# Performance work log

Hardware: AMD Instinct MI355X
Metric: run time of the kernel (lower is better)

## Reference

```python
import jax, jax.numpy as jnp
import numpy as np

EMBED_DIM = 1024
NUM_HEADS = 16
HEAD_DIM = EMBED_DIM // NUM_HEADS
FF_DIM = 4096
B, T, S = 2, 2048, 2048
LN_EPS = 1e-5


def setup_inputs() -> dict:
    key = jax.random.key(0)
    ks = jax.random.split(key, 20)
    sd = 1.0 / np.sqrt(EMBED_DIM)
    d = {
        'x': jax.random.normal(ks[0], (B, T, EMBED_DIM), jnp.float32),
        'encoder_outputs': jax.random.normal(ks[1], (B, S, EMBED_DIM), jnp.float32),
        'tgt_mask': jnp.tril(jnp.ones((T, T), bool))[None, None],  # [1,1,T,T] causal
    }
    # weights stored [in, out] so y = x @ W + b
    names = ['sa_wq', 'sa_wk', 'sa_wv', 'sa_wo', 'ca_wq', 'ca_wk', 'ca_wv', 'ca_wo']
    for i, n in enumerate(names):
        d[n] = jax.random.normal(ks[2 + i], (EMBED_DIM, EMBED_DIM), jnp.float32) * sd
        d[n.replace('w', 'b')] = jnp.zeros((EMBED_DIM,), jnp.float32)
    d['ff_w1'] = jax.random.normal(ks[10], (EMBED_DIM, FF_DIM), jnp.float32) * sd
    d['ff_b1'] = jnp.zeros((FF_DIM,), jnp.float32)
    d['ff_w2'] = jax.random.normal(ks[11], (FF_DIM, EMBED_DIM), jnp.float32) * (1.0 / np.sqrt(FF_DIM))
    d['ff_b2'] = jnp.zeros((EMBED_DIM,), jnp.float32)
    for i in (1, 2, 3):
        d[f'ln{i}_g'] = jnp.ones((EMBED_DIM,), jnp.float32)
        d[f'ln{i}_b'] = jnp.zeros((EMBED_DIM,), jnp.float32)
    return d


def _layernorm(x, g, b):
    mu = jnp.mean(x, -1, keepdims=True)
    var = jnp.mean(jnp.square(x - mu), -1, keepdims=True)
    return (x - mu) * jax.lax.rsqrt(var + LN_EPS) * g + b


def _mha(q_in, k_in, v_in, wq, bq, wk, bk, wv, bv, wo, bo, mask=None):
    Bq, Tq, C = q_in.shape
    Tk = k_in.shape[1]
    Q = (q_in @ wq + bq).reshape(Bq, Tq, NUM_HEADS, HEAD_DIM)
    K = (k_in @ wk + bk).reshape(Bq, Tk, NUM_HEADS, HEAD_DIM)
    V = (v_in @ wv + bv).reshape(Bq, Tk, NUM_HEADS, HEAD_DIM)
    scores = jnp.einsum('bqhd,bkhd->bhqk', Q, K) / np.sqrt(HEAD_DIM)
    if mask is not None:
        scores = jnp.where(mask, scores, -jnp.inf)
    attn = jax.nn.softmax(scores, axis=-1)
    out = jnp.einsum('bhqk,bkhd->bqhd', attn, V).reshape(Bq, Tq, C)
    return out @ wo + bo


def reference(x, encoder_outputs, tgt_mask,
              sa_wq, sa_bq, sa_wk, sa_bk, sa_wv, sa_bv, sa_wo, sa_bo,
              ca_wq, ca_bq, ca_wk, ca_bk, ca_wv, ca_bv, ca_wo, ca_bo,
              ff_w1, ff_b1, ff_w2, ff_b2,
              ln1_g, ln1_b, ln2_g, ln2_b, ln3_g, ln3_b):
    h = _layernorm(x, ln1_g, ln1_b)
    x = x + _mha(h, h, h, sa_wq, sa_bq, sa_wk, sa_bk, sa_wv, sa_bv, sa_wo, sa_bo, tgt_mask)
    h = _layernorm(x, ln2_g, ln2_b)
    x = x + _mha(h, encoder_outputs, encoder_outputs,
                 ca_wq, ca_bq, ca_wk, ca_bk, ca_wv, ca_bv, ca_wo, ca_bo, None)
    h = _layernorm(x, ln3_g, ln3_b)
    ff = jax.nn.relu(h @ ff_w1 + ff_b1) @ ff_w2 + ff_b2
    return x + ff
```

## Files before the change

kernel.cpp:

```cpp
#include <hip/hip_runtime.h>
#include <stdint.h>


typedef __bf16 bf16x8 __attribute__((ext_vector_type(8)));
typedef float  f32x4  __attribute__((ext_vector_type(4)));

#define T_SEQ 2048
#define NROWS 4096
#define QSCALE 0.18033688011112042f

__device__ __forceinline__ unsigned short f2bf(float f) {
  union { float f; unsigned int u; } v; v.f = f;
  unsigned int u = v.u;
  return (unsigned short)((u + 0x7FFFu + ((u >> 16) & 1u)) >> 16);
}
__device__ __forceinline__ float bf2f(unsigned short h) {
  union { unsigned int u; float f; } v; v.u = ((unsigned int)h) << 16;
  return v.f;
}
__device__ __forceinline__ unsigned int pk2(float a, float b) {
  return (unsigned int)f2bf(a) | ((unsigned int)f2bf(b) << 16);
}
__device__ __forceinline__ unsigned int pk2t(float a, float b) {
  union { float f; unsigned int u; } ua, ub;
  ua.f = a; ub.f = b;
  return __builtin_amdgcn_perm(ub.u, ua.u, 0x07060302u);
}
__device__ __forceinline__ float fexp2(float x) {
  return __builtin_amdgcn_exp2f(x);
}
union U4 { unsigned int u[4]; bf16x8 v; };

__global__ void probe_dtype_kernel(const unsigned short* __restrict__ p,
                                   int* __restrict__ flag) {
  __shared__ int cnt;
  if (threadIdx.x == 0) cnt = 0;
  __syncthreads();
  int bad = 0;
  for (int i = threadIdx.x; i < 4096; i += 256) {
    unsigned short u = p[i];
    int e = (u >> 7) & 0xFF;
    if (u != 0 && (e < 100 || e > 140)) bad++;
  }
  atomicAdd(&cnt, bad);
  __syncthreads();
  if (threadIdx.x == 0) *flag = (cnt < 512) ? 1 : 0;
}

struct WTbl {
  const void* src[10];
  int K[10], N[10], start[10];
  unsigned int dstoff[10];
};
__global__ void wtrans_fused_kernel(WTbl tbl, unsigned short* __restrict__ wsbase,
                                    const int* __restrict__ flag) {
  __shared__ unsigned short tile[32][33];
  const int lb = blockIdx.x;
  int wi = 0;
#pragma unroll
  for (int i = 1; i < 10; i++) wi = (lb >= tbl.start[i]) ? i : wi;
  const int local = lb - tbl.start[wi];
  const int Nw = tbl.N[wi], Kw = tbl.K[wi];
  const int bx = local & ((Nw >> 5) - 1);
  const int by = local / (Nw >> 5);
  const void* W = tbl.src[wi];
  unsigned short* Wt = wsbase + tbl.dstoff[wi];
  const int n0 = bx * 32, k0 = by * 32;
  const int c = threadIdx.x & 31, r0 = threadIdx.x >> 5;
  const bool isbf = (*flag != 0);
  for (int r = r0; r < 32; r += 8) {
    unsigned short v;
    if (isbf) v = ((const unsigned short*)W)[(size_t)(k0 + r) * Nw + n0 + c];
    else      v = f2bf(((const float*)W)[(size_t)(k0 + r) * Nw + n0 + c]);
    tile[r][c] = v;
  }
  __syncthreads();
  const bool packed = (wi == 3) || (wi >= 7);
  if (!packed) {
    for (int r = r0; r < 32; r += 8)
      Wt[(size_t)(n0 + r) * Kw + k0 + c] = tile[c][r];
  } else {
    const int k = k0 + c;
    const size_t kpart = ((size_t)(k >> 5) << 9) + ((((k >> 3) & 3) << 7) + (k & 7));
    const size_t kfr = (size_t)(Kw >> 5);
    for (int r = r0; r < 32; r += 8) {
      const int n = n0 + r;
      Wt[((size_t)(n >> 4) * kfr << 9) + kpart + ((n & 15) << 3)] = tile[c][r];
    }
  }
}

struct PTbl { const void* p[19]; };
__global__ void param_cvt_kernel(PTbl tbl, float* __restrict__ out,
                                 const int* __restrict__ flag) {
  const int blk = blockIdx.x;
  const int off = (blk >= 8 && blk < 12) ? (blk - 8) * 1024 : 0;
  const void* src = tbl.p[blk];
  const int i = threadIdx.x * 4;
  float4 o;
  if (*flag) {
    const unsigned short* u = (const unsigned short*)src + off;
    ushort4 q = *(const ushort4*)&u[i];
    o.x = bf2f(q.x); o.y = bf2f(q.y); o.z = bf2f(q.z); o.w = bf2f(q.w);
  } else {
    o = *(const float4*)&((const float*)src)[off + i];
  }
  *(float4*)&out[blk * 1024 + i] = o;
}

__global__ void cvt_to_bf16_kernel(const void* __restrict__ in,
                                   unsigned short* __restrict__ out,
                                   int n, const int* __restrict__ flag) {
  int i = (blockIdx.x * 256 + threadIdx.x) * 8;
  if (i >= n) return;
  if (*flag) {
    *(int4*)&out[i] = *(const int4*)&((const unsigned short*)in)[i];
  } else {
    const float* f = (const float*)in;
    float4 a = *(const float4*)&f[i];
    float4 c = *(const float4*)&f[i + 4];
    ushort4 o1, o2;
    o1.x = f2bf(a.x); o1.y = f2bf(a.y); o1.z = f2bf(a.z); o1.w = f2bf(a.w);
    o2.x = f2bf(c.x); o2.y = f2bf(c.y); o2.z = f2bf(c.z); o2.w = f2bf(c.w);
    *(ushort4*)&out[i] = o1;
    *(ushort4*)&out[i + 4] = o2;
  }
}

__global__ void cvt_to_f32_kernel(const void* __restrict__ in,
                                  float* __restrict__ out,
                                  int n, const int* __restrict__ flag) {
  int i = (blockIdx.x * 256 + threadIdx.x) * 4;
  if (i >= n) return;
  if (*flag) {
    const unsigned short* u = (const unsigned short*)in;
    ushort4 q = *(const ushort4*)&u[i];
    float4 o;
    o.x = bf2f(q.x); o.y = bf2f(q.y); o.z = bf2f(q.z); o.w = bf2f(q.w);
    *(float4*)&out[i] = o;
  } else {
    *(float4*)&out[i] = *(const float4*)&((const float*)in)[i];
  }
}

__global__ __launch_bounds__(256) void ln_kernel(
    const float* __restrict__ x, const float* __restrict__ g,
    const float* __restrict__ b, unsigned short* __restrict__ out) {
  const int row = blockIdx.x;
  const int t = threadIdx.x;
  const size_t base = (size_t)row * 1024;
  float4 v = *(const float4*)&x[base + t * 4];
  float s1 = v.x + v.y + v.z + v.w;
  float s2 = v.x * v.x + v.y * v.y + v.z * v.z + v.w * v.w;
#pragma unroll
  for (int d = 1; d < 64; d <<= 1) {
    s1 += __shfl_xor(s1, d, 64);
    s2 += __shfl_xor(s2, d, 64);
  }
  __shared__ float a1[4], a2[4];
  if ((t & 63) == 0) { a1[t >> 6] = s1; a2[t >> 6] = s2; }
  __syncthreads();
  s1 = a1[0] + a1[1] + a1[2] + a1[3];
  s2 = a2[0] + a2[1] + a2[2] + a2[3];
  const float mean = s1 * (1.0f / 1024.0f);
  const float var = s2 * (1.0f / 1024.0f) - mean * mean;
  const float rstd = rsqrtf(fmaxf(var, 0.0f) + 1e-5f);
  float4 gv = *(const float4*)&g[t * 4];
  float4 bv = *(const float4*)&b[t * 4];
  ushort4 o;
  o.x = f2bf((v.x - mean) * rstd * gv.x + bv.x);
  o.y = f2bf((v.y - mean) * rstd * gv.y + bv.y);
  o.z = f2bf((v.z - mean) * rstd * gv.z + bv.z);
  o.w = f2bf((v.w - mean) * rstd * gv.w + bv.w);
  *(ushort4*)&out[base + t * 4] = o;
}

template <int BM, int BN, int BK, int RELU, int RESID, int OUTM,
          int BIASROW, int SCALEMODE>
__global__ __launch_bounds__(256, 2) void gemm_kernel(
    const unsigned short* __restrict__ A, const unsigned short* __restrict__ Bt,
    const float* __restrict__ bias, const float* __restrict__ resid,
    void* __restrict__ outp, int M, int N, int K,
    const int* __restrict__ flag) {
  static_assert(BK == 64, "swizzle assumes 8 chunks/row");
  constexpr int WX = (BN == 64) ? 1 : 2;
  constexpr int WY = 4 / WX;
  constexpr int WM = BM / WY, WN = BN / WX;
  constexpr int MI = WM / 16, NJ = WN / 16;
  constexpr int ACALLS = BM * BK / 2048;
  constexpr int RPC = 2048 / BK;
  __shared__ unsigned short lsA[2][BM * BK];
  const int t = threadIdx.x;
  const int wave = t >> 6, lane = t & 63;
  const int ml = lane & 15, quad = lane >> 4;
  const int cx = ml & 7;
  const int wm = (wave / WX) * WM, wn = (wave % WX) * WN;

  const int nx = gridDim.x, ny = gridDim.y;
  const int lin = (int)blockIdx.y * nx + (int)blockIdx.x;
  const int per = 8 * nx;
  const int y0 = (lin / per) * 8;
  const int gsz = (ny - y0 < 8) ? (ny - y0) : 8;
  const int by = y0 + (lin % gsz);
  const int bx = (lin % per) / gsz;
  const size_t m0 = (size_t)by * BM;
  const size_t n0 = (size_t)bx * BN;

  f32x4 acc[MI][NJ];
  const f32x4 fz = {0.f, 0.f, 0.f, 0.f};
#pragma unroll
  for (int i = 0; i < MI; i++)
#pragma unroll
    for (int j = 0; j < NJ; j++) acc[i][j] = fz;

  const int rowL = t >> 3;
  const int colL = (((t & 7) ^ ((t >> 3) & 7)) * 8);
  const unsigned short* gA = A + (m0 + rowL) * (size_t)K + colL;
  const int kfr = K >> 5;
  const unsigned short* gBp =
      Bt + ((size_t)((n0 + wn) >> 4) * kfr) * 512 + lane * 8;

  auto stageA = [&](unsigned short* dA, int k0) {
#pragma unroll
    for (int c = 0; c < ACALLS; c++)
      __builtin_amdgcn_global_load_lds(
          (const __attribute__((address_space(1))) void*)(gA + (size_t)(c * RPC) * K + k0),
          (__attribute__((address_space(3))) void*)(dA + c * 2048 + wave * 512), 16, 0, 0);
  };
  auto loadB = [&](bf16x8 (&bq)[NJ][2], int k0) {
#pragma unroll
    for (int j = 0; j < NJ; j++)
#pragma unroll
      for (int h = 0; h < 2; h++)
        bq[j][h] = *(const bf16x8*)(gBp + ((size_t)j * kfr + (k0 >> 5) + h) * 512);
  };
  auto comp = [&](const unsigned short* bA, const bf16x8 (&bq)[NJ][2]) {
#pragma unroll
    for (int h = 0; h < 2; h++) {
      bf16x8 af[MI];
#pragma unroll
      for (int i = 0; i < MI; i++)
        af[i] = *(const bf16x8*)
            &bA[(wm + i * 16 + ml) * BK + (((h * 4 + quad) ^ cx) * 8)];
#pragma unroll
      for (int i = 0; i < MI; i++)
#pragma unroll
        for (int j = 0; j < NJ; j++)
          acc[i][j] = __builtin_amdgcn_mfma_f32_16x16x32_bf16(af[i], bq[j][h],
                                                              acc[i][j], 0, 0, 0);
    }
  };

  const int nk = K / BK;
  bf16x8 bq0[NJ][2], bq1[NJ][2];
  stageA(&lsA[0][0], 0);
  loadB(bq0, 0);
  int tk = 0;
  while (tk < nk) {
    asm volatile("s_waitcnt vmcnt(0)" ::: "memory");
    __builtin_amdgcn_s_barrier();
    if (tk + 1 < nk) { stageA(&lsA[1][0], (tk + 1) * BK); loadB(bq1, (tk + 1) * BK); }
    comp(&lsA[0][0], bq0);
    if (tk + 1 < nk) {
      asm volatile("s_waitcnt vmcnt(0)" ::: "memory");
      __builtin_amdgcn_s_barrier();
      if (tk + 2 < nk) { stageA(&lsA[0][0], (tk + 2) * BK); loadB(bq0, (tk + 2) * BK); }
      comp(&lsA[1][0], bq1);
    }
    tk += 2;
  }

  const bool obf = (OUTM == 1) || (OUTM == 2 && *flag != 0);
#pragma unroll
  for (int j = 0; j < NJ; j++) {
    const size_t cg = n0 + wn + j * 16 + ml;
    const float bcol = BIASROW ? 0.0f : bias[cg];
    const float sc = (SCALEMODE == 0) ? 1.0f
                   : (SCALEMODE == 1) ? QSCALE
                                      : (cg < 1024 ? QSCALE : 1.0f);
#pragma unroll
    for (int i = 0; i < MI; i++) {
#pragma unroll
      for (int r = 0; r < 4; r++) {
        const size_t rg = m0 + wm + i * 16 + quad * 4 + r;
        const float bval = BIASROW ? bias[rg] : bcol;
        float v = (acc[i][j][r] + bval) * sc;
        if (RELU) v = fmaxf(v, 0.0f);
        if (RESID) v += resid[rg * N + cg];
        if (obf) ((unsigned short*)outp)[rg * N + cg] = f2bf(v);
        else     ((float*)outp)[rg * N + cg] = v;
      }
    }
  }
}

struct GSeg {
  const unsigned short* A; const unsigned short* B;
  const float* bias; unsigned short* out;
  int N, K, start, gxlog2, mode;
};
template <int NSEG>
__global__ __launch_bounds__(256, 4) void gemm_multi_kernel(GSeg s0, GSeg s1,
                                                            GSeg s2) {
  constexpr int BM = 128, BN = 64, BK = 64;
  constexpr int WM = 32, WN = 64;
  constexpr int MI = 2, NJ = 4;
  __shared__ unsigned short lsA[BM * BK];
  __shared__ unsigned short lsB[BN * BK];
  const int blk = (int)blockIdx.x;
  GSeg sg = s0;
  if (NSEG > 1 && blk >= s1.start) sg = s1;
  if (NSEG > 2 && blk >= s2.start) sg = s2;
  const int t = threadIdx.x;
  const int wave = t >> 6, lane = t & 63;
  const int ml = lane & 15, quad = lane >> 4;
  const int cx = ml & 7;
  const int wm = wave * WM, wn = 0;
  const int N = sg.N, K = sg.K;

  const int lin = blk - sg.start;
  const int per = 8 << sg.gxlog2;
  const int y0 = (lin / per) * 8;
  const int by = y0 + (lin & 7);
  const int bx = (lin & (per - 1)) >> 3;
  const size_t m0 = (size_t)by * BM;
  const size_t n0 = (size_t)bx * BN;

  f32x4 acc[MI][NJ];
  const f32x4 fz = {0.f, 0.f, 0.f, 0.f};
#pragma unroll
  for (int i = 0; i < MI; i++)
#pragma unroll
    for (int j = 0; j < NJ; j++) acc[i][j] = fz;

  const int rowL = t >> 3;
  const int colL = (((t & 7) ^ ((t >> 3) & 7)) * 8);
  const unsigned short* gA = sg.A + (m0 + rowL) * (size_t)K + colL;
  const unsigned short* gB = sg.B + (n0 + rowL) * (size_t)K + colL;

  for (int k0 = 0; k0 < K; k0 += BK) {
    __syncthreads();
#pragma unroll
    for (int c = 0; c < 4; c++)
      __builtin_amdgcn_global_load_lds(
          (const __attribute__((address_space(1))) void*)(gA + (size_t)(c * 32) * K + k0),
          (__attribute__((address_space(3))) void*)&lsA[c * 2048 + wave * 512], 16, 0, 0);
#pragma unroll
    for (int c = 0; c < 2; c++)
      __builtin_amdgcn_global_load_lds(
          (const __attribute__((address_space(1))) void*)(gB + (size_t)(c * 32) * K + k0),
          (__attribute__((address_space(3))) void*)&lsB[c * 2048 + wave * 512], 16, 0, 0);
    __syncthreads();
#pragma unroll
    for (int h = 0; h < BK / 32; h++) {
      bf16x8 af[MI], bfv[NJ];
#pragma unroll
      for (int i = 0; i < MI; i++)
        af[i] = *(const bf16x8*)
            &lsA[(wm + i * 16 + ml) * BK + (((h * 4 + quad) ^ cx) * 8)];
#pragma unroll
      for (int j = 0; j < NJ; j++)
        bfv[j] = *(const bf16x8*)
            &lsB[(wn + j * 16 + ml) * BK + (((h * 4 + quad) ^ cx) * 8)];
#pragma unroll
      for (int i = 0; i < MI; i++)
#pragma unroll
        for (int j = 0; j < NJ; j++)
          acc[i][j] = __builtin_amdgcn_mfma_f32_16x16x32_bf16(af[i], bfv[j],
                                                              acc[i][j], 0, 0, 0);
    }
  }

  const int mode = sg.mode;
#pragma unroll
  for (int j = 0; j < NJ; j++) {
    const size_t cg = n0 + wn + j * 16 + ml;
    const float bcol = (mode & 1) ? 0.0f : sg.bias[cg];
    const float sc = (mode & 2) ? QSCALE
                   : ((mode & 4) && cg < 1024) ? QSCALE : 1.0f;
#pragma unroll
    for (int i = 0; i < MI; i++) {
#pragma unroll
      for (int r = 0; r < 4; r++) {
        const size_t rg = m0 + wm + i * 16 + quad * 4 + r;
        const float bval = (mode & 1) ? sg.bias[rg] : bcol;
        float v = (acc[i][j][r] + bval) * sc;
        sg.out[rg * N + cg] = f2bf(v);
      }
    }
  }
}

template <int CAUSAL>
__global__ __launch_bounds__(256, 4) void attn_kernel(
    const unsigned short* __restrict__ Q, const unsigned short* __restrict__ K,
    const unsigned short* __restrict__ VT, unsigned short* __restrict__ O,
    int qstride, int kstride) {
  __shared__ unsigned short Ks[4096];
  __shared__ unsigned short Vs[4096];
  __shared__ unsigned short Qs[4608];
  const int t = threadIdx.x;
  const int wave = t >> 6, lane = t & 63;
  const int ml = lane & 15, quad = lane >> 4;
  const int cx = ml & 7;
  const int bh = blockIdx.y, b = bh >> 4, h = bh & 15;
  const int qb = CAUSAL ? ((int)gridDim.x - 1 - (int)blockIdx.x) : (int)blockIdx.x;
  const int q0 = qb * 64;
  const int lr = lane >> 3;
  const int scol = (((lane & 7) ^ lr) * 8);

  {
    const unsigned short* g0 =
        Q + ((size_t)(b * T_SEQ + q0 + wave * 16 + lr)) * qstride + h * 64 + scol;
    __builtin_amdgcn_global_load_lds(
        (const __attribute__((address_space(1))) void*)g0,
        (__attribute__((address_space(3))) void*)&Qs[wave * 2 * 512], 16, 0, 0);
    const unsigned short* g1 = g0 + (size_t)8 * qstride;
    __builtin_amdgcn_global_load_lds(
        (const __attribute__((address_space(1))) void*)g1,
        (__attribute__((address_space(3))) void*)&Qs[(wave * 2 + 1) * 512], 16, 0, 0);
  }

  int sp_[2];
#pragma unroll
  for (int i = 0; i < 2; i++) {
    int p = (wave * 2 + i) * 8 + lr;
    sp_[i] = ((p & 16) << 1) | ((p & 12) << 1) | ((p & 32) >> 3) | (p & 3);
  }
  const unsigned short* kg0 =
      K + ((size_t)b * T_SEQ + sp_[0]) * kstride + h * 64 + scol;
  const unsigned short* kg1 =
      K + ((size_t)b * T_SEQ + sp_[1]) * kstride + h * 64 + scol;
  const unsigned short* vg0 =
      VT + ((size_t)(h * 64 + wave * 16 + lr)) * 4096 + (size_t)b * T_SEQ + scol;
  const unsigned short* vg1 = vg0 + (size_t)8 * 4096;

  __syncthreads();
  const bf16x8 aq0 = *(const bf16x8*)&Qs[(wave * 16 + ml) * 64 + ((quad ^ cx) * 8)];
  const bf16x8 aq1 = *(const bf16x8*)&Qs[(wave * 16 + ml) * 64 + (((quad + 4) ^ cx) * 8)];

  f32x4 acc[4];
  const f32x4 fz = {0.f, 0.f, 0.f, 0.f};
#pragma unroll
  for (int n = 0; n < 4; n++) acc[n] = fz;
  float m_i = -3.0e38f, l_part = 0.0f;
  const int q_glob = q0 + wave * 16 + ml;
  const int nkb = CAUSAL ? (qb + 1) : (T_SEQ / 64);
  const size_t kinc = (size_t)64 * kstride;

  for (int kb = 0; kb < nkb; kb++) {
    __syncthreads();
    __builtin_amdgcn_global_load_lds(
        (const __attribute__((address_space(1))) void*)kg0,
        (__attribute__((address_space(3))) void*)&Ks[(wave * 2) * 512], 16, 0, 0);
    __builtin_amdgcn_global_load_lds(
        (const __attribute__((address_space(1))) void*)kg1,
        (__attribute__((address_space(3))) void*)&Ks[(wave * 2 + 1) * 512], 16, 0, 0);
    __builtin_amdgcn_global_load_lds(
        (const __attribute__((address_space(1))) void*)vg0,
        (__attribute__((address_space(3))) void*)&Vs[(wave * 2) * 512], 16, 0, 0);
    __builtin_amdgcn_global_load_lds(
        (const __attribute__((address_space(1))) void*)vg1,
        (__attribute__((address_space(3))) void*)&Vs[(wave * 2 + 1) * 512], 16, 0, 0);
    kg0 += kinc; kg1 += kinc; vg0 += 64; vg1 += 64;
    __syncthreads();

    f32x4 s[4];
#pragma unroll
    for (int nt = 0; nt < 4; nt++) {
      bf16x8 k0 = *(const bf16x8*)&Ks[(nt * 16 + ml) * 64 + ((quad ^ cx) * 8)];
      bf16x8 k1 = *(const bf16x8*)&Ks[(nt * 16 + ml) * 64 + (((quad + 4) ^ cx) * 8)];
      f32x4 a = fz;
      a = __builtin_amdgcn_mfma_f32_16x16x32_bf16(k0, aq0, a, 0, 0, 0);
      a = __builtin_amdgcn_mfma_f32_16x16x32_bf16(k1, aq1, a, 0, 0, 0);
      s[nt] = a;
    }
    if (CAUSAL && kb == nkb - 1) {
#pragma unroll
      for (int nt = 0; nt < 4; nt++)
#pragma unroll
        for (int r = 0; r < 4; r++) {
          int key = kb * 64 + ((nt & 1) << 5) + (quad << 3) + ((nt >> 1) << 2) + r;
          if (key > q_glob) s[nt][r] = -3.0e38f;
        }
    }
    float tm = -3.0e38f;
#pragma unroll
    for (int nt = 0; nt < 4; nt++)
#pragma unroll
      for (int r = 0; r < 4; r++) tm = fmaxf(tm, s[nt][r]);
    tm = fmaxf(tm, __shfl_xor(tm, 16));
    tm = fmaxf(tm, __shfl_xor(tm, 32));
    if (__any(tm > m_i)) {
      const float m_new = fmaxf(m_i, tm);
      const float alpha = fexp2(m_i - m_new);
      l_part *= alpha;
#pragma unroll
      for (int n = 0; n < 4; n++)
#pragma unroll
        for (int r = 0; r < 4; r++) acc[n][r] *= alpha;
      m_i = m_new;
    }
    float p[4][4];
    float rs = 0.f;
#pragma unroll
    for (int nt = 0; nt < 4; nt++)
#pragma unroll
      for (int r = 0; r < 4; r++) {
        p[nt][r] = fexp2(s[nt][r] - m_i);
        rs += p[nt][r];
      }
    l_part += rs;

    U4 P0, P1;
    P0.u[0] = pk2t(p[0][0], p[0][1]); P0.u[1] = pk2t(p[0][2], p[0][3]);
    P0.u[2] = pk2t(p[2][0], p[2][1]); P0.u[3] = pk2t(p[2][2], p[2][3]);
    P1.u[0] = pk2t(p[1][0], p[1][1]); P1.u[1] = pk2t(p[1][2], p[1][3]);
    P1.u[2] = pk2t(p[3][0], p[3][1]); P1.u[3] = pk2t(p[3][2], p[3][3]);

#pragma unroll
    for (int n = 0; n < 4; n++) {
      bf16x8 v0 = *(const bf16x8*)&Vs[(n * 16 + ml) * 64 + ((quad ^ cx) * 8)];
      bf16x8 v1 = *(const bf16x8*)&Vs[(n * 16 + ml) * 64 + (((quad + 4) ^ cx) * 8)];
      acc[n] = __builtin_amdgcn_mfma_f32_16x16x32_bf16(v0, P0.v, acc[n], 0, 0, 0);
      acc[n] = __builtin_amdgcn_mfma_f32_16x16x32_bf16(v1, P1.v, acc[n], 0, 0, 0);
    }
  }

  float l_i = l_part;
  l_i += __shfl_xor(l_i, 16);
  l_i += __shfl_xor(l_i, 32);

  const float inv = 1.0f / l_i;
#pragma unroll
  for (int n = 0; n < 4; n++)
#pragma unroll
    for (int rp = 0; rp < 2; rp++) {
      unsigned int u = pk2(acc[n][2 * rp] * inv, acc[n][2 * rp + 1] * inv);
      *(unsigned int*)&Qs[(wave * 16 + ml) * 72 + n * 16 + quad * 4 + 2 * rp] = u;
    }
  __syncthreads();
  {
    const int q = t >> 2, d0 = (t & 3) * 16;
    unsigned short* og = O + ((size_t)(b * T_SEQ + q0 + q)) * 1024 + h * 64 + d0;
    *(int4*)og = *(const int4*)&Qs[q * 72 + d0];
    *(int4*)(og + 8) = *(const int4*)&Qs[q * 72 + d0 + 8];
  }
}

extern "C" void kernel_launch(void* const* d_in, const int* in_sizes, int n_in,
                              void* d_out, int out_size, void* d_ws,
                              size_t ws_size, hipStream_t stream) {
  (void)in_sizes; (void)n_in; (void)out_size; (void)ws_size;
  const size_t MEG = 1048576;
  unsigned short* ws16 = (unsigned short*)d_ws;
  char* wsb = (char*)d_ws;

  unsigned short* wt[10];
  for (int i = 0; i < 8; i++) wt[i] = ws16 + (size_t)i * MEG;
  wt[8] = ws16 + 8 * MEG;
  wt[9] = ws16 + 12 * MEG;
  unsigned short* encB  = ws16 + 16 * MEG;
  unsigned short* hbuf  = ws16 + 20 * MEG;
  unsigned short* QKb   = ws16 + 24 * MEG;
  unsigned short* Qb    = ws16 + 32 * MEG;
  unsigned short* Kb    = ws16 + 36 * MEG;
  unsigned short* Vb    = ws16 + 40 * MEG;
  unsigned short* attnb = ws16 + 44 * MEG;
  unsigned short* ffh   = ws16 + 24 * MEG;
  float* xf32 = (float*)(wsb + 96 * MEG);
  float* pbuf = (float*)(wsb + 112 * MEG);
  int* flag   = (int*)(wsb + 113 * MEG);

  probe_dtype_kernel<<<1, 256, 0, stream>>>((const unsigned short*)d_in[0], flag);

  {
    WTbl tb;
    const int widx[10] = {3, 5, 7, 9, 11, 13, 15, 17, 19, 21};
    int st = 0;
    for (int i = 0; i < 10; i++) {
      tb.src[i] = d_in[widx[i]];
      tb.K[i] = (i == 9) ? 4096 : 1024;
      tb.N[i] = (i == 8) ? 4096 : 1024;
      tb.start[i] = st;
      st += (tb.K[i] / 32) * (tb.N[i] / 32);
      tb.dstoff[i] = (unsigned int)((i < 8) ? i * MEG : (i == 8 ? 8 * MEG : 12 * MEG));
    }
    wtrans_fused_kernel<<<16384, 256, 0, stream>>>(tb, ws16, flag);
  }

  cvt_to_f32_kernel<<<4096, 256, 0, stream>>>(d_in[0], xf32, 4194304, flag);
  cvt_to_bf16_kernel<<<2048, 256, 0, stream>>>(d_in[1], encB, 4194304, flag);

  {
    PTbl pt;
    const int pidx[19] = {4, 6, 8, 10, 12, 14, 16, 18,
                          20, 20, 20, 20, 22, 23, 24, 25, 26, 27, 28};
    for (int i = 0; i < 19; i++) pt.p[i] = d_in[pidx[i]];
    param_cvt_kernel<<<19, 256, 0, stream>>>(pt, pbuf, flag);
  }
  float* bqk_sa = pbuf;
  float* bv_sa  = pbuf + 2048;
  float* bo_sa  = pbuf + 3072;
  float* bq_ca  = pbuf + 4096;
  float* bk_ca  = pbuf + 5120;
  float* bv_ca  = pbuf + 6144;
  float* bo_ca  = pbuf + 7168;
  float* ff_b1p = pbuf + 8192;
  float* ff_b2p = pbuf + 12288;
  float* ln1g = pbuf + 13312; float* ln1b = pbuf + 14336;
  float* ln2g = pbuf + 15360; float* ln2b = pbuf + 16384;
  float* ln3g = pbuf + 17408; float* ln3b = pbuf + 18432;

  dim3 gP(16, 32);
  dim3 gFF1(32, 32);
  dim3 gFF2(8, 64);
  dim3 gAttn(32, 32);

  ln_kernel<<<4096, 256, 0, stream>>>(xf32, ln1g, ln1b, hbuf);
  {
    GSeg sQK = {hbuf, wt[0], bqk_sa, QKb, 2048, 1024, 0, 5, 4};
    GSeg sVT = {wt[2], hbuf, bv_sa, Vb, 4096, 1024, 1024, 6, 1};
    gemm_multi_kernel<2><<<1536, 256, 0, stream>>>(sQK, sVT, sVT);
  }
  attn_kernel<1><<<gAttn, 256, 0, stream>>>(QKb, QKb + 1024, Vb, attnb, 2048, 2048);
  gemm_kernel<128, 64, 64, 0, 1, 0, 0, 0><<<gP, 256, 0, stream>>>(
      attnb, wt[3], bo_sa, xf32, xf32, NROWS, 1024, 1024, nullptr);

  ln_kernel<<<4096, 256, 0, stream>>>(xf32, ln2g, ln2b, hbuf);
  {
    GSeg sQ = {hbuf, wt[4], bq_ca, Qb, 1024, 1024, 0, 4, 2};
    GSeg sK = {encB, wt[5], bk_ca, Kb, 1024, 1024, 512, 4, 0};
    GSeg sV = {wt[6], encB, bv_ca, Vb, 4096, 1024, 1024, 6, 1};
    gemm_multi_kernel<3><<<1536, 256, 0, stream>>>(sQ, sK, sV);
  }
  attn_kernel<0><<<gAttn, 256, 0, stream>>>(Qb, Kb, Vb, attnb, 1024, 1024);
  gemm_kernel<128, 64, 64, 0, 1, 0, 0, 0><<<gP, 256, 0, stream>>>(
      attnb, wt[7], bo_ca, xf32, xf32, NROWS, 1024, 1024, nullptr);

  ln_kernel<<<4096, 256, 0, stream>>>(xf32, ln3g, ln3b, hbuf);
  gemm_kernel<128, 128, 64, 1, 0, 1, 0, 0><<<gFF1, 256, 0, stream>>>(
      hbuf, wt[8], ff_b1p, nullptr, ffh, NROWS, 4096, 1024, nullptr);
  gemm_kernel<64, 128, 64, 0, 1, 2, 0, 0><<<gFF2, 256, 0, stream>>>(
      ffh, wt[9], ff_b2p, xf32, d_out, NROWS, 1024, 4096, flag);
}
```

Before: 577.3 us.

## Double-buffer attention K/V tiles, split-K the FF2 GEMM, lazy softmax rescale

The attention kernel now double-buffers its K and V tiles in LDS, so loads for the next key block are issued before the current block is computed. The epilogue reuses the K buffer, which lets the Q staging area shrink. The online-softmax rescale now runs only when the running max grows by more than 8, cutting how often rescaling happens. Separately, FF2 is split along K into two halves that write fp32 partials, and a new combine kernel adds the partials, bias and residual. This doubles FF2 parallelism at the cost of extra partial-buffer traffic and one more launch.

Result: faster. 564.6 us (-2.2%).

```diff
diff --git a/kernel.cpp b/kernel.cpp
--- a/kernel.cpp
+++ b/kernel.cpp
@@ -176,12 +176,12 @@
 }
 
 template <int BM, int BN, int BK, int RELU, int RESID, int OUTM,
-          int BIASROW, int SCALEMODE>
+          int BIASROW, int SCALEMODE, int SPLITK>
 __global__ __launch_bounds__(256, 2) void gemm_kernel(
     const unsigned short* __restrict__ A, const unsigned short* __restrict__ Bt,
     const float* __restrict__ bias, const float* __restrict__ resid,
     void* __restrict__ outp, int M, int N, int K,
-    const int* __restrict__ flag) {
+    const int* __restrict__ flag, void* __restrict__ outp2) {
   static_assert(BK == 64, "swizzle assumes 8 chunks/row");
   constexpr int WX = (BN == 64) ? 1 : 2;
   constexpr int WY = 4 / WX;
@@ -251,23 +251,40 @@
     }
   };
 
-  const int nk = K / BK;
+  const int kbase = SPLITK ? (int)blockIdx.z * (K >> 1) : 0;
+  const int nk = (SPLITK ? (K >> 1) : K) / BK;
   bf16x8 bq0[NJ][2], bq1[NJ][2];
-  stageA(&lsA[0][0], 0);
-  loadB(bq0, 0);
+  stageA(&lsA[0][0], kbase);
+  loadB(bq0, kbase);
   int tk = 0;
   while (tk < nk) {
     asm volatile("s_waitcnt vmcnt(0)" ::: "memory");
     __builtin_amdgcn_s_barrier();
-    if (tk + 1 < nk) { stageA(&lsA[1][0], (tk + 1) * BK); loadB(bq1, (tk + 1) * BK); }
+    if (tk + 1 < nk) { stageA(&lsA[1][0], kbase + (tk + 1) * BK); loadB(bq1, kbase + (tk + 1) * BK); }
     comp(&lsA[0][0], bq0);
     if (tk + 1 < nk) {
       asm volatile("s_waitcnt vmcnt(0)" ::: "memory");
       __builtin_amdgcn_s_barrier();
-      if (tk + 2 < nk) { stageA(&lsA[0][0], (tk + 2) * BK); loadB(bq0, (tk + 2) * BK); }
+      if (tk + 2 < nk) { stageA(&lsA[0][0], kbase + (tk + 2) * BK); loadB(bq0, kbase + (tk + 2) * BK); }
       comp(&lsA[1][0], bq1);
     }
     tk += 2;
+  }
+
+  if constexpr (SPLITK) {
+    float* po = (blockIdx.z == 0) ? (float*)outp : (float*)outp2;
+#pragma unroll
+    for (int j = 0; j < NJ; j++) {
+      const size_t cg = n0 + wn + j * 16 + ml;
+#pragma unroll
+      for (int i = 0; i < MI; i++)
+#pragma unroll
+        for (int r = 0; r < 4; r++) {
+          const size_t rg = m0 + wm + i * 16 + quad * 4 + r;
+          po[rg * N + cg] = acc[i][j][r];
+        }
+    }
+    return;
   }
 
   const bool obf = (OUTM == 1) || (OUTM == 2 && *flag != 0);
@@ -291,6 +308,31 @@
         else     ((float*)outp)[rg * N + cg] = v;
       }
     }
+  }
+}
+
+__global__ __launch_bounds__(256) void ff2_combine_kernel(
+    const float* __restrict__ p0, const float* __restrict__ p1,
+    const float* __restrict__ bias, const float* __restrict__ resid,
+    void* __restrict__ out, const int* __restrict__ flag) {
+  const int row = blockIdx.x;
+  const int i = threadIdx.x * 4;
+  const size_t off = (size_t)row * 1024 + i;
+  float4 a = *(const float4*)&p0[off];
+  float4 b = *(const float4*)&p1[off];
+  float4 r = *(const float4*)&resid[off];
+  float4 bb = *(const float4*)&bias[i];
+  float4 v;
+  v.x = a.x + b.x + bb.x + r.x;
+  v.y = a.y + b.y + bb.y + r.y;
+  v.z = a.z + b.z + bb.z + r.z;
+  v.w = a.w + b.w + bb.w + r.w;
+  if (*flag) {
+    ushort4 o;
+    o.x = f2bf(v.x); o.y = f2bf(v.y); o.z = f2bf(v.z); o.w = f2bf(v.w);
+    *(ushort4*)&((unsigned short*)out)[off] = o;
+  } else {
+    *(float4*)&((float*)out)[off] = v;
   }
 }
 
@@ -396,9 +438,9 @@
     const unsigned short* __restrict__ Q, const unsigned short* __restrict__ K,
     const unsigned short* __restrict__ VT, unsigned short* __restrict__ O,
     int qstride, int kstride) {
-  __shared__ unsigned short Ks[4096];
-  __shared__ unsigned short Vs[4096];
-  __shared__ unsigned short Qs[4608];
+  __shared__ unsigned short Ks[2][4096];
+  __shared__ unsigned short Vs[2][4096];
+  __shared__ unsigned short Qs[4096];
   const int t = threadIdx.x;
   const int wave = t >> 6, lane = t & 63;
   const int ml = lane & 15, quad = lane >> 4;
@@ -434,6 +476,7 @@
   const unsigned short* vg0 =
       VT + ((size_t)(h * 64 + wave * 16 + lr)) * 4096 + (size_t)b * T_SEQ + scol;
   const unsigned short* vg1 = vg0 + (size_t)8 * 4096;
+  const size_t kinc = (size_t)64 * kstride;
 
   __syncthreads();
   const bf16x8 aq0 = *(const bf16x8*)&Qs[(wave * 16 + ml) * 64 + ((quad ^ cx) * 8)];
@@ -446,30 +489,29 @@
   float m_i = -3.0e38f, l_part = 0.0f;
   const int q_glob = q0 + wave * 16 + ml;
   const int nkb = CAUSAL ? (qb + 1) : (T_SEQ / 64);
-  const size_t kinc = (size_t)64 * kstride;
-
-  for (int kb = 0; kb < nkb; kb++) {
-    __syncthreads();
+
+  auto stage = [&](unsigned short* kdst, unsigned short* vdst) {
     __builtin_amdgcn_global_load_lds(
         (const __attribute__((address_space(1))) void*)kg0,
-        (__attribute__((address_space(3))) void*)&Ks[(wave * 2) * 512], 16, 0, 0);
+        (__attribute__((address_space(3))) void*)(kdst + (wave * 2) * 512), 16, 0, 0);
     __builtin_amdgcn_global_load_lds(
         (const __attribute__((address_space(1))) void*)kg1,
-        (__attribute__((address_space(3))) void*)&Ks[(wave * 2 + 1) * 512], 16, 0, 0);
+        (__attribute__((address_space(3))) void*)(kdst + (wave * 2 + 1) * 512), 16, 0, 0);
     __builtin_amdgcn_global_load_lds(
         (const __attribute__((address_space(1))) void*)vg0,
-        (__attribute__((address_space(3))) void*)&Vs[(wave * 2) * 512], 16, 0, 0);
+        (__attribute__((address_space(3))) void*)(vdst + (wave * 2) * 512), 16, 0, 0);
     __builtin_amdgcn_global_load_lds(
         (const __attribute__((address_space(1))) void*)vg1,
-        (__attribute__((address_space(3))) void*)&Vs[(wave * 2 + 1) * 512], 16, 0, 0);
+        (__attribute__((address_space(3))) void*)(vdst + (wave * 2 + 1) * 512), 16, 0, 0);
     kg0 += kinc; kg1 += kinc; vg0 += 64; vg1 += 64;
-    __syncthreads();
-
+  };
+
+  auto compute = [&](const unsigned short* Kb, const unsigned short* Vb, int kb) {
     f32x4 s[4];
 #pragma unroll
     for (int nt = 0; nt < 4; nt++) {
-      bf16x8 k0 = *(const bf16x8*)&Ks[(nt * 16 + ml) * 64 + ((quad ^ cx) * 8)];
-      bf16x8 k1 = *(const bf16x8*)&Ks[(nt * 16 + ml) * 64 + (((quad + 4) ^ cx) * 8)];
+      bf16x8 k0 = *(const bf16x8*)&Kb[(nt * 16 + ml) * 64 + ((quad ^ cx) * 8)];
+      bf16x8 k1 = *(const bf16x8*)&Kb[(nt * 16 + ml) * 64 + (((quad + 4) ^ cx) * 8)];
       f32x4 a = fz;
       a = __builtin_amdgcn_mfma_f32_16x16x32_bf16(k0, aq0, a, 0, 0, 0);
       a = __builtin_amdgcn_mfma_f32_16x16x32_bf16(k1, aq1, a, 0, 0, 0);
@@ -491,7 +533,7 @@
       for (int r = 0; r < 4; r++) tm = fmaxf(tm, s[nt][r]);
     tm = fmaxf(tm, __shfl_xor(tm, 16));
     tm = fmaxf(tm, __shfl_xor(tm, 32));
-    if (__any(tm > m_i)) {
+    if (__any(tm > m_i + 8.0f)) {
       const float m_new = fmaxf(m_i, tm);
       const float alpha = fexp2(m_i - m_new);
       l_part *= alpha;
@@ -520,10 +562,24 @@
 
 #pragma unroll
     for (int n = 0; n < 4; n++) {
-      bf16x8 v0 = *(const bf16x8*)&Vs[(n * 16 + ml) * 64 + ((quad ^ cx) * 8)];
-      bf16x8 v1 = *(const bf16x8*)&Vs[(n * 16 + ml) * 64 + (((quad + 4) ^ cx) * 8)];
+      bf16x8 v0 = *(const bf16x8*)&Vb[(n * 16 + ml) * 64 + ((quad ^ cx) * 8)];
+      bf16x8 v1 = *(const bf16x8*)&Vb[(n * 16 + ml) * 64 + (((quad + 4) ^ cx) * 8)];
       acc[n] = __builtin_amdgcn_mfma_f32_16x16x32_bf16(v0, P0.v, acc[n], 0, 0, 0);
       acc[n] = __builtin_amdgcn_mfma_f32_16x16x32_bf16(v1, P1.v, acc[n], 0, 0, 0);
+    }
+  };
+
+  stage(&Ks[0][0], &Vs[0][0]);
+  for (int kb = 0; kb < nkb; kb += 2) {
+    asm volatile("s_waitcnt vmcnt(0)" ::: "memory");
+    __syncthreads();
+    if (kb + 1 < nkb) stage(&Ks[1][0], &Vs[1][0]);
+    compute(&Ks[0][0], &Vs[0][0], kb);
+    if (kb + 1 < nkb) {
+      asm volatile("s_waitcnt vmcnt(0)" ::: "memory");
+      __syncthreads();
+      if (kb + 2 < nkb) stage(&Ks[0][0], &Vs[0][0]);
+      compute(&Ks[1][0], &Vs[1][0], kb + 1);
     }
   }
 
@@ -531,20 +587,22 @@
   l_i += __shfl_xor(l_i, 16);
   l_i += __shfl_xor(l_i, 32);
 
+  __syncthreads();
+  unsigned short* eps = &Ks[0][0];
   const float inv = 1.0f / l_i;
 #pragma unroll
   for (int n = 0; n < 4; n++)
 #pragma unroll
     for (int rp = 0; rp < 2; rp++) {
       unsigned int u = pk2(acc[n][2 * rp] * inv, acc[n][2 * rp + 1] * inv);
-      *(unsigned int*)&Qs[(wave * 16 + ml) * 72 + n * 16 + quad * 4 + 2 * rp] = u;
+      *(unsigned int*)&eps[(wave * 16 + ml) * 72 + n * 16 + quad * 4 + 2 * rp] = u;
     }
   __syncthreads();
   {
     const int q = t >> 2, d0 = (t & 3) * 16;
     unsigned short* og = O + ((size_t)(b * T_SEQ + q0 + q)) * 1024 + h * 64 + d0;
-    *(int4*)og = *(const int4*)&Qs[q * 72 + d0];
-    *(int4*)(og + 8) = *(const int4*)&Qs[q * 72 + d0 + 8];
+    *(int4*)og = *(const int4*)&eps[q * 72 + d0];
+    *(int4*)(og + 8) = *(const int4*)&eps[q * 72 + d0 + 8];
   }
 }
 
@@ -571,6 +629,8 @@
   float* xf32 = (float*)(wsb + 96 * MEG);
   float* pbuf = (float*)(wsb + 112 * MEG);
   int* flag   = (int*)(wsb + 113 * MEG);
+  float* part0 = (float*)(wsb + 32 * MEG);
+  float* part1 = (float*)(wsb + 80 * MEG);
 
   probe_dtype_kernel<<<1, 256, 0, stream>>>((const unsigned short*)d_in[0], flag);
 
@@ -614,7 +674,7 @@
 
   dim3 gP(16, 32);
   dim3 gFF1(32, 32);
-  dim3 gFF2(8, 64);
+  dim3 gFF2(8, 64, 2);
   dim3 gAttn(32, 32);
 
   ln_kernel<<<4096, 256, 0, stream>>>(xf32, ln1g, ln1b, hbuf);
@@ -624,8 +684,8 @@
     gemm_multi_kernel<2><<<1536, 256, 0, stream>>>(sQK, sVT, sVT);
   }
   attn_kernel<1><<<gAttn, 256, 0, stream>>>(QKb, QKb + 1024, Vb, attnb, 2048, 2048);
-  gemm_kernel<128, 64, 64, 0, 1, 0, 0, 0><<<gP, 256, 0, stream>>>(
-      attnb, wt[3], bo_sa, xf32, xf32, NROWS, 1024, 1024, nullptr);
+  gemm_kernel<128, 64, 64, 0, 1, 0, 0, 0, 0><<<gP, 256, 0, stream>>>(
+      attnb, wt[3], bo_sa, xf32, xf32, NROWS, 1024, 1024, nullptr, nullptr);
 
   ln_kernel<<<4096, 256, 0, stream>>>(xf32, ln2g, ln2b, hbuf);
   {
@@ -635,12 +695,14 @@
     gemm_multi_kernel<3><<<1536, 256, 0, stream>>>(sQ, sK, sV);
   }
   attn_kernel<0><<<gAttn, 256, 0, stream>>>(Qb, Kb, Vb, attnb, 1024, 1024);
-  gemm_kernel<128, 64, 64, 0, 1, 0, 0, 0><<<gP, 256, 0, stream>>>(
-      attnb, wt[7], bo_ca, xf32, xf32, NROWS, 1024, 1024, nullptr);
+  gemm_kernel<128, 64, 64, 0, 1, 0, 0, 0, 0><<<gP, 256, 0, stream>>>(
+      attnb, wt[7], bo_ca, xf32, xf32, NROWS, 1024, 1024, nullptr, nullptr);
 
   ln_kernel<<<4096, 256, 0, stream>>>(xf32, ln3g, ln3b, hbuf);
-  gemm_kernel<128, 128, 64, 1, 0, 1, 0, 0><<<gFF1, 256, 0, stream>>>(
-      hbuf, wt[8], ff_b1p, nullptr, ffh, NROWS, 4096, 1024, nullptr);
-  gemm_kernel<64, 128, 64, 0, 1, 2, 0, 0><<<gFF2, 256, 0, stream>>>(
-      ffh, wt[9], ff_b2p, xf32, d_out, NROWS, 1024, 4096, flag);
-}
+  gemm_kernel<128, 128, 64, 1, 0, 1, 0, 0, 0><<<gFF1, 256, 0, stream>>>(
+      hbuf, wt[8], ff_b1p, nullptr, ffh, NROWS, 4096, 1024, nullptr, nullptr);
+  gemm_kernel<64, 128, 64, 0, 0, 0, 0, 0, 1><<<gFF2, 256, 0, stream>>>(
+      ffh, wt[9], nullptr, nullptr, part0, NROWS, 1024, 4096, flag, part1);
+  ff2_combine_kernel<<<4096, 256, 0, stream>>>(part0, part1, ff_b2p, xf32,
+                                               d_out, flag);
+}
```
